# Optimization experiments

Hardware: AMD Instinct MI355X
Metric: run time of the kernel (lower is better)

Reference implementation:

```python
import jax, jax.numpy as jnp
import numpy as np

# Static graph layout: B equal-sized graphs of N nodes, DEG random edges per node.
B, N, DEG = 128, 1024, 16
F_IN, H, C = 2, 64, 2
RATIO = 0.8
E = B * N * DEG
K1 = int(np.ceil(RATIO * N))      # 820
K2 = int(np.ceil(RATIO * K1))     # 656
K3 = int(np.ceil(RATIO * K2))     # 525


def setup_inputs() -> dict:
    key = jax.random.key(0)
    ks = jax.random.split(key, 24)
    x = jax.random.normal(ks[0], (B * N, F_IN), jnp.float32)
    edge_attr = jax.random.uniform(ks[1], (E,), jnp.float32)
    # per-graph random endpoints, offset so edges stay inside each graph
    local = jax.random.randint(ks[2], (2, B, N * DEG), 0, N)
    edge_index = (local + (jnp.arange(B) * N)[None, :, None]).reshape(2, E)

    def lin(k, i, o):
        return jax.random.normal(k, (i, o), jnp.float32) / np.sqrt(i)

    def bias(k, o):
        return jax.random.normal(k, (o,), jnp.float32) * 0.01

    return {
        "x": x, "edge_attr": edge_attr,
        "W1": lin(ks[3], F_IN, H), "b1": bias(ks[4], H),
        "Wp1": lin(ks[5], H, 1), "bp1": bias(ks[6], 1),
        "W2": lin(ks[7], H, H), "b2": bias(ks[8], H),
        "Wp2": lin(ks[9], H, 1), "bp2": bias(ks[10], 1),
        "W3": lin(ks[11], H, H), "b3": bias(ks[12], H),
        "Wp3": lin(ks[13], H, 1), "bp3": bias(ks[14], 1),
        "Wl1": lin(ks[15], 2 * H, H), "bl1": bias(ks[16], H),
        "Wl2": lin(ks[17], H, H // 2), "bl2": bias(ks[18], H // 2),
        "Wl3": lin(ks[19], H // 2, C), "bl3": bias(ks[20], C),
        "edge_index": edge_index,
    }


def gcn(x, src, dst, w, W, b):
    """PyG GCNConv with gcn_norm (self-loops weight 1)."""
    h = x @ W                                       # [BN, out]
    deg = jnp.zeros((x.shape[0],), x.dtype).at[dst].add(w) + 1.0
    dinv = jax.lax.rsqrt(deg)
    norm = dinv[src] * w * dinv[dst]                # [E]
    out = jnp.zeros_like(h).at[dst].add(norm[:, None] * h[src])
    out = out + (dinv * dinv)[:, None] * h          # self-loop term
    return out + b


def sagpool(x, alive, src, dst, Wp, bp, k):
    """SAGPool: unweighted GCN scoring, per-graph top-k, x <- x * tanh(score).
    Removed nodes/edges are kept as masked (alive=False) slots -> static shapes."""
    we = (alive[src] & alive[dst]).astype(x.dtype)
    score = gcn(x, src, dst, we, Wp, bp)[:, 0]      # [BN]
    s = jnp.where(alive, score, -jnp.inf).reshape(B, N)
    _, idx = jax.lax.top_k(s, k)                    # [B, k]
    alive_new = jnp.zeros((B, N), bool).at[jnp.arange(B)[:, None], idx].set(True).reshape(-1)
    xn = jnp.where(alive_new[:, None], x * jnp.tanh(score)[:, None], 0.0)
    return xn, alive_new


def readout(x, alive):
    """concat(global_max_pool, global_mean_pool) over alive nodes per graph."""
    xr = x.reshape(B, N, -1)
    m = alive.reshape(B, N, 1)
    mx = jnp.max(jnp.where(m, xr, -jnp.inf), axis=1)
    mn = jnp.sum(jnp.where(m, xr, 0.0), axis=1) / jnp.sum(m, axis=1).astype(x.dtype)
    return jnp.concatenate([mx, mn], axis=1)        # [B, 2*H]


def _forward(x, edge_attr, W1, b1, Wp1, bp1, W2, b2, Wp2, bp2, W3, b3, Wp3, bp3,
             Wl1, bl1, Wl2, bl2, Wl3, bl3, edge_index):
    src, dst = edge_index[0], edge_index[1]
    h = jax.nn.relu(gcn(x, src, dst, edge_attr, W1, b1))
    h, a1 = sagpool(h, jnp.ones((B * N,), bool), src, dst, Wp1, bp1, K1)
    x1 = readout(h, a1)

    ea1 = edge_attr * (a1[src] & a1[dst]).astype(x.dtype)
    h = jax.nn.relu(gcn(h, src, dst, ea1, W2, b2))
    h, a2 = sagpool(h, a1, src, dst, Wp2, bp2, K2)
    x2 = readout(h, a2)

    # conv3 is called WITHOUT edge_weight -> surviving edges get weight 1
    ea2 = (a2[src] & a2[dst]).astype(x.dtype)
    h = jax.nn.relu(gcn(h, src, dst, ea2, W3, b3))
    h, a3 = sagpool(h, a2, src, dst, Wp3, bp3, K3)
    x3 = readout(h, a3)

    g = x1 + x2 + x3
    g = jax.nn.relu(g @ Wl1 + bl1)                  # dropout: eval mode (identity)
    g = jax.nn.relu(g @ Wl2 + bl2)
    return jax.nn.log_softmax(g @ Wl3 + bl3, axis=-1)


def reference(x, edge_attr, W1, b1, Wp1, bp1, W2, b2, Wp2, bp2, W3, b3, Wp3, bp3,
              Wl1, bl1, Wl2, bl2, Wl3, bl3, edge_index):
    return _forward(x, edge_attr, W1, b1, Wp1, bp1, W2, b2, Wp2, bp2, W3, b3,
                    Wp3, bp3, Wl1, bl1, Wl2, bl2, Wl3, bl3, edge_index)
```

## Files before the change

### kernel.cpp

```cpp
#include <hip/hip_runtime.h>
#include <math.h>

#define NB 128
#define NN 1024
#define BNODES (NB*NN)
#define NE 2097152
#define EPG (NE/NB)
#define EPT (EPG/NN)
#define FH 64
#define KK1 820
#define KK2 656
#define KK3 525

__global__ __launch_bounds__(1024) void k_csr(const int* __restrict__ ei,
                                              const float* __restrict__ ea,
                                              int* __restrict__ rowptr,
                                              int2* __restrict__ csr_sw,
                                              int* __restrict__ aliveA,
                                              float* __restrict__ dinvW,
                                              float* __restrict__ dinvU) {
  extern __shared__ int2 lcsr[];
  __shared__ int cnt[NN];
  __shared__ int cur[NN];
  __shared__ float wsum[NN];
  int b = blockIdx.x, t = threadIdx.x;
  int node = b*NN + t;
  aliveA[node] = 1;
  cnt[t] = 0;
  wsum[t] = 0.f;
  __syncthreads();
  int ebase = b*EPG;
  int se[EPT]; int de[EPT]; float we[EPT];
  #pragma unroll
  for (int i = 0; i < EPT; ++i) {
    int e = ebase + i*NN + t;
    se[i] = ei[e];
    de[i] = ei[NE + e] - b*NN;
    we[i] = ea[e];
    atomicAdd(&cnt[de[i]], 1);
    atomicAdd(&wsum[de[i]], we[i]);
  }
  __syncthreads();
  int v = cnt[t];
  for (int off = 1; off < NN; off <<= 1) {
    int u = (t >= off) ? cnt[t - off] : 0;
    __syncthreads();
    cnt[t] += u;
    __syncthreads();
  }
  int excl = cnt[t] - v;
  rowptr[node] = ebase + excl;
  cur[t] = excl;
  dinvW[node] = rsqrtf(1.f + wsum[t]);
  dinvU[node] = rsqrtf(1.f + (float)v);
  if (b == NB-1 && t == NN-1) rowptr[BNODES] = NE;
  __syncthreads();
  #pragma unroll
  for (int i = 0; i < EPT; ++i) {
    int pos = atomicAdd(&cur[de[i]], 1);
    lcsr[pos] = make_int2(se[i], __float_as_int(we[i]));
  }
  __syncthreads();
  float4* dst4 = (float4*)(csr_sw + ebase);
  const float4* src4 = (const float4*)lcsr;
  #pragma unroll
  for (int i = 0; i < EPG/2/NN; ++i)
    dst4[i*NN + t] = src4[i*NN + t];
}

template<int MODE>
__global__ void k_degs(const int* __restrict__ rowptr, const int2* __restrict__ csr_sw,
                       const int* __restrict__ alive,
                       float* __restrict__ dinvW, float* __restrict__ dinvU) {
  int t = threadIdx.x;
  int l16 = t & 15;
  int d = blockIdx.x*16 + (t >> 4);
  int r0 = rowptr[d], r1 = rowptr[d+1];
  float sW = 0.f, sU = 0.f;
  for (int base = r0; base < r1; base += 16) {
    if (base + l16 < r1) {
      int2 p = csr_sw[base + l16];
      if (alive[p.x]) { sW += (MODE == 2) ? 1.f : __int_as_float(p.y); sU += 1.f; }
    }
  }
  #pragma unroll
  for (int off = 8; off; off >>= 1) {
    sW += __shfl_xor(sW, off, 16);
    sU += __shfl_xor(sU, off, 16);
  }
  if (l16 == 0) {
    bool dA = (alive[d] != 0);
    dinvW[d] = dA ? rsqrtf(1.f + sW) : 0.f;
    dinvU[d] = dA ? rsqrtf(1.f + sU) : 0.f;
  }
}

__global__ void k_lin1(const float* __restrict__ x, const float* __restrict__ W,
                       float* __restrict__ h) {
  int i = blockIdx.x*256 + threadIdx.x;
  if (i >= BNODES*FH) return;
  int node = i >> 6, f = i & 63;
  h[i] = x[2*node]*W[f] + x[2*node+1]*W[FH + f];
}

__global__ void k_lin64(const float* __restrict__ hA, const float* __restrict__ tm,
                        const float* __restrict__ W, float* __restrict__ hB) {
  __shared__ float sX[64][65];
  __shared__ float sW[64*64];
  int t = threadIdx.x;
  for (int i = t; i < 1024; i += 256) ((float4*)sW)[i] = ((const float4*)W)[i];
  int nb = blockIdx.x * 64;
  #pragma unroll
  for (int i = 0; i < 16; ++i) {
    int gidx = (nb << 6) + i*256 + t;
    int node = gidx >> 6, f = gidx & 63;
    sX[node - nb][f] = hA[gidx] * tm[node];
  }
  __syncthreads();
  int node = t >> 2;
  int f0 = (t & 3) * 16;
  float4 a0 = {0,0,0,0}, a1 = a0, a2 = a0, a3 = a0;
  #pragma unroll 4
  for (int k = 0; k < 64; ++k) {
    float xv = sX[node][k];
    const float4 w0 = *(const float4*)&sW[k*64 + f0];
    const float4 w1 = *(const float4*)&sW[k*64 + f0 + 4];
    const float4 w2 = *(const float4*)&sW[k*64 + f0 + 8];
    const float4 w3 = *(const float4*)&sW[k*64 + f0 + 12];
    a0.x = fmaf(xv, w0.x, a0.x); a0.y = fmaf(xv, w0.y, a0.y);
    a0.z = fmaf(xv, w0.z, a0.z); a0.w = fmaf(xv, w0.w, a0.w);
    a1.x = fmaf(xv, w1.x, a1.x); a1.y = fmaf(xv, w1.y, a1.y);
    a1.z = fmaf(xv, w1.z, a1.z); a1.w = fmaf(xv, w1.w, a1.w);
    a2.x = fmaf(xv, w2.x, a2.x); a2.y = fmaf(xv, w2.y, a2.y);
    a2.z = fmaf(xv, w2.z, a2.z); a2.w = fmaf(xv, w2.w, a2.w);
    a3.x = fmaf(xv, w3.x, a3.x); a3.y = fmaf(xv, w3.y, a3.y);
    a3.z = fmaf(xv, w3.z, a3.z); a3.w = fmaf(xv, w3.w, a3.w);
  }
  float4* dst = (float4*)(hB + (size_t)(nb + node)*FH + f0);
  dst[0] = a0; dst[1] = a1; dst[2] = a2; dst[3] = a3;
}

template<int MODE>
__global__ __launch_bounds__(1024) void k_gath(
    const int* __restrict__ rowptr, const int2* __restrict__ csr_sw,
    const float* __restrict__ dinvW, const float* __restrict__ hB,
    const float* __restrict__ bias, const float* __restrict__ Wp,
    float* __restrict__ hA, float* __restrict__ qpart) {
  extern __shared__ float sHB[];
  __shared__ float sDW[NN];
  __shared__ float sWp[32];
  __shared__ float sB[32];
  int b = blockIdx.x >> 1, half = blockIdx.x & 1;
  int t = threadIdx.x, l8 = t & 7;
  int gbase = b*NN;
  sDW[t] = dinvW[gbase + t];
  if (t < 32) { sWp[t] = Wp[half*32 + t]; sB[t] = bias[half*32 + t]; }
  const float4* hB4 = (const float4*)hB;
  float4* sHB4 = (float4*)sHB;
  #pragma unroll
  for (int i = 0; i < 8; ++i) {
    int idx = i*1024 + t;
    int n = idx >> 3, j = idx & 7;
    sHB4[n*8 + j] = hB4[(size_t)(gbase + n)*16 + half*8 + j];
  }
  __syncthreads();
  float4 bv = ((const float4*)sB)[l8];
  float4 wp = ((const float4*)sWp)[l8];
  #pragma unroll 1
  for (int pass = 0; pass < 8; ++pass) {
    int n = pass*128 + (t >> 3);
    int gn = gbase + n;
    float dd = sDW[n];
    float4 hv = sHB4[n*8 + l8];
    float dd2 = dd*dd;
    float4 acc;
    acc.x = fmaf(dd2, hv.x, bv.x);
    acc.y = fmaf(dd2, hv.y, bv.y);
    acc.z = fmaf(dd2, hv.z, bv.z);
    acc.w = fmaf(dd2, hv.w, bv.w);
    int r0 = rowptr[gn], r1 = rowptr[gn+1];
    for (int base = r0; base < r1; base += 8) {
      int sj = 0; float cj = 0.f;
      if (base + l8 < r1) {
        int2 p = csr_sw[base + l8];
        sj = p.x - gbase;
        float w = (MODE == 2) ? 1.f : __int_as_float(p.y);
        cj = sDW[sj] * w * dd;
      }
      #pragma unroll
      for (int j = 0; j < 8; ++j) {
        int s   = __shfl(sj, j, 8);
        float c = __shfl(cj, j, 8);
        float4 v = sHB4[s*8 + l8];
        acc.x = fmaf(c, v.x, acc.x);
        acc.y = fmaf(c, v.y, acc.y);
        acc.z = fmaf(c, v.z, acc.z);
        acc.w = fmaf(c, v.w, acc.w);
      }
    }
    acc.x = fmaxf(acc.x, 0.f); acc.y = fmaxf(acc.y, 0.f);
    acc.z = fmaxf(acc.z, 0.f); acc.w = fmaxf(acc.w, 0.f);
    ((float4*)hA)[(size_t)gn*16 + half*8 + l8] = acc;
    float dot = acc.x*wp.x + acc.y*wp.y + acc.z*wp.z + acc.w*wp.w;
    dot += __shfl_xor(dot, 4, 8);
    dot += __shfl_xor(dot, 2, 8);
    dot += __shfl_xor(dot, 1, 8);
    if (l8 == 0) qpart[half*BNODES + gn] = dot;
  }
}

__global__ void k_qfin(const float* __restrict__ dinvU, const float* __restrict__ qp,
                       float* __restrict__ q) {
  int i = blockIdx.x*256 + threadIdx.x;
  if (i < BNODES) q[i] = dinvU[i]*(qp[i] + qp[BNODES + i]);
}

__global__ void k_score(const int* __restrict__ rowptr, const int2* __restrict__ csr_sw,
                        const float* __restrict__ dinvU, const float* __restrict__ q,
                        const float* __restrict__ bp, float* __restrict__ score) {
  int t = threadIdx.x;
  int l16 = t & 15;
  int d = blockIdx.x*16 + (t >> 4);
  float du = dinvU[d];
  float sum = 0.f;
  if (du != 0.f) {
    int r0 = rowptr[d], r1 = rowptr[d+1];
    for (int base = r0; base < r1; base += 16)
      if (base + l16 < r1) sum += q[csr_sw[base + l16].x];
  }
  #pragma unroll
  for (int off = 8; off; off >>= 1) sum += __shfl_xor(sum, off, 16);
  if (l16 == 0) score[d] = bp[0] + du*(q[d] + sum);
}

__global__ void k_topk(const float* __restrict__ score,
                       const int* __restrict__ alive, int k,
                       float* __restrict__ tm, int* __restrict__ aliveNext) {
  __shared__ float sc[NN];
  int b = blockIdx.x >> 2, p = blockIdx.x & 3;
  int t = threadIdx.x;
  int gbase = b*NN;
  #pragma unroll
  for (int i = 0; i < 4; ++i) {
    int n = i*256 + t;
    sc[n] = alive[gbase + n] ? score[gbase + n] : -INFINITY;
  }
  __syncthreads();
  int n = p*256 + t;
  int node = gbase + n;
  float me = sc[n];
  float raw = score[node];
  int rank = 0;
  const float4* sc4 = (const float4*)sc;
  for (int j4 = 0; j4 < NN/4; ++j4) {
    float4 o = sc4[j4];
    int jb = j4*4;
    rank += (o.x > me) || (o.x == me && jb+0 < n);
    rank += (o.y > me) || (o.y == me && jb+1 < n);
    rank += (o.z > me) || (o.z == me && jb+2 < n);
    rank += (o.w > me) || (o.w == me && jb+3 < n);
  }
  int sel = (rank < k) ? 1 : 0;
  aliveNext[node] = sel;
  tm[node] = sel ? tanhf(raw) : 0.f;
}

__global__ void k_sread(const float* __restrict__ hA, const float* __restrict__ tm,
                        const int* __restrict__ aliveN,
                        float* __restrict__ pmax, float* __restrict__ psum) {
  __shared__ float rm[4][FH], rs[4][FH];
  int b = blockIdx.x >> 2, p = blockIdx.x & 3;
  int t = threadIdx.x, f = t & 63, r = t >> 6;
  float mx = -INFINITY, sm = 0.f;
  for (int i = 0; i < 64; ++i) {
    int n = p*256 + i*4 + r;
    int node = b*NN + n;
    float v = hA[(size_t)node*FH + f] * tm[node];
    if (aliveN[node]) { mx = fmaxf(mx, v); sm += v; }
  }
  rm[r][f] = mx; rs[r][f] = sm;
  __syncthreads();
  if (t < FH) {
    float m2 = fmaxf(fmaxf(rm[0][t], rm[1][t]), fmaxf(rm[2][t], rm[3][t]));
    float s2 = rs[0][t] + rs[1][t] + rs[2][t] + rs[3][t];
    pmax[(b*4 + p)*FH + t] = m2;
    psum[(b*4 + p)*FH + t] = s2;
  }
}

__global__ void k_mlp(const float* __restrict__ pmax, const float* __restrict__ psum,
                      const float* __restrict__ Wl1, const float* __restrict__ bl1,
                      const float* __restrict__ Wl2, const float* __restrict__ bl2,
                      const float* __restrict__ Wl3, const float* __restrict__ bl3,
                      float* __restrict__ out) {
  __shared__ float sg[2*FH];
  __shared__ float l1[FH];
  __shared__ float l2[FH/2];
  __shared__ float l3[2];
  int b = blockIdx.x, t = threadIdx.x;
  const float kf[3] = {(float)KK1, (float)KK2, (float)KK3};
  float gm = 0.f, gs = 0.f;
  #pragma unroll
  for (int l = 0; l < 3; ++l) {
    const float* pm = pmax + (size_t)l*NB*4*FH + (b*4)*FH;
    const float* ps = psum + (size_t)l*NB*4*FH + (b*4)*FH;
    float mm = -INFINITY, ss = 0.f;
    #pragma unroll
    for (int p = 0; p < 4; ++p) {
      mm = fmaxf(mm, pm[p*FH + t]);
      ss += ps[p*FH + t];
    }
    gm += mm;
    gs += ss / kf[l];
  }
  sg[t] = gm;
  sg[FH + t] = gs;
  __syncthreads();
  float acc = bl1[t];
  #pragma unroll
  for (int k = 0; k < 2*FH; ++k) acc = fmaf(sg[k], Wl1[k*FH + t], acc);
  l1[t] = fmaxf(acc, 0.f);
  __syncthreads();
  if (t < 32) {
    float a2 = bl2[t];
    #pragma unroll
    for (int k = 0; k < FH; ++k) a2 = fmaf(l1[k], Wl2[k*32 + t], a2);
    l2[t] = fmaxf(a2, 0.f);
  }
  __syncthreads();
  if (t < 2) {
    float a3 = bl3[t];
    #pragma unroll
    for (int k = 0; k < 32; ++k) a3 = fmaf(l2[k], Wl3[k*2 + t], a3);
    l3[t] = a3;
  }
  __syncthreads();
  if (t == 0) {
    float m = fmaxf(l3[0], l3[1]);
    float lse = m + logf(expf(l3[0]-m) + expf(l3[1]-m));
    out[b*2+0] = l3[0] - lse;
    out[b*2+1] = l3[1] - lse;
  }
}

extern "C" void kernel_launch(void* const* d_in, const int* in_sizes, int n_in,
                              void* d_out, int out_size, void* d_ws, size_t ws_size,
                              hipStream_t stream) {
  const float* x   = (const float*)d_in[0];
  const float* ea  = (const float*)d_in[1];
  const float* W1  = (const float*)d_in[2];
  const float* b1  = (const float*)d_in[3];
  const float* Wp1 = (const float*)d_in[4];
  const float* bp1 = (const float*)d_in[5];
  const float* W2  = (const float*)d_in[6];
  const float* b2  = (const float*)d_in[7];
  const float* Wp2 = (const float*)d_in[8];
  const float* bp2 = (const float*)d_in[9];
  const float* W3  = (const float*)d_in[10];
  const float* b3  = (const float*)d_in[11];
  const float* Wp3 = (const float*)d_in[12];
  const float* bp3 = (const float*)d_in[13];
  const float* Wl1 = (const float*)d_in[14];
  const float* bl1 = (const float*)d_in[15];
  const float* Wl2 = (const float*)d_in[16];
  const float* bl2 = (const float*)d_in[17];
  const float* Wl3 = (const float*)d_in[18];
  const float* bl3 = (const float*)d_in[19];
  const int*   ei  = (const int*)d_in[20];
  float* out = (float*)d_out;

  int2* csr_sw = (int2*)d_ws;
  float* hA    = (float*)(csr_sw + NE);
  float* hB    = hA + (size_t)BNODES*FH;
  float* dinvW = hB + (size_t)BNODES*FH;
  float* dinvU = dinvW + BNODES;
  float* q     = dinvU + BNODES;
  float* qpart = q + BNODES;
  float* score = qpart + 2*BNODES;
  float* tm    = score + BNODES;
  float* pmax  = tm + BNODES;
  float* psum  = pmax + 3*NB*4*FH;
  int* aliveA  = (int*)(psum + 3*NB*4*FH);
  int* aliveB  = aliveA + BNODES;
  int* rowptr  = aliveB + BNODES;

  const int TB = 256;
  const int gG  = BNODES / 16;
  const int gNH = BNODES*FH / TB;
  const int gL  = BNODES / 64;
  const int gN  = BNODES / TB;
  const size_t gathLds = (size_t)NN*32*sizeof(float);

  k_csr<<<NB, 1024, EPG*sizeof(int2), stream>>>(ei, ea, rowptr, csr_sw, aliveA,
                                                dinvW, dinvU);

  k_lin1<<<gNH, TB, 0, stream>>>(x, W1, hB);
  k_gath<0><<<NB*2, 1024, gathLds, stream>>>(rowptr, csr_sw, dinvW, hB, b1, Wp1, hA, qpart);
  k_qfin<<<gN, TB, 0, stream>>>(dinvU, qpart, q);
  k_score<<<gG, TB, 0, stream>>>(rowptr, csr_sw, dinvU, q, bp1, score);
  k_topk<<<NB*4, TB, 0, stream>>>(score, aliveA, KK1, tm, aliveB);
  k_sread<<<NB*4, TB, 0, stream>>>(hA, tm, aliveB, pmax, psum);

  k_degs<1><<<gG, TB, 0, stream>>>(rowptr, csr_sw, aliveB, dinvW, dinvU);
  k_lin64<<<gL, TB, 0, stream>>>(hA, tm, W2, hB);
  k_gath<1><<<NB*2, 1024, gathLds, stream>>>(rowptr, csr_sw, dinvW, hB, b2, Wp2, hA, qpart);
  k_qfin<<<gN, TB, 0, stream>>>(dinvU, qpart, q);
  k_score<<<gG, TB, 0, stream>>>(rowptr, csr_sw, dinvU, q, bp2, score);
  k_topk<<<NB*4, TB, 0, stream>>>(score, aliveB, KK2, tm, aliveA);
  k_sread<<<NB*4, TB, 0, stream>>>(hA, tm, aliveA, pmax + NB*4*FH, psum + NB*4*FH);

  k_degs<2><<<gG, TB, 0, stream>>>(rowptr, csr_sw, aliveA, dinvW, dinvU);
  k_lin64<<<gL, TB, 0, stream>>>(hA, tm, W3, hB);
  k_gath<2><<<NB*2, 1024, gathLds, stream>>>(rowptr, csr_sw, dinvW, hB, b3, Wp3, hA, qpart);
  k_qfin<<<gN, TB, 0, stream>>>(dinvU, qpart, q);
  k_score<<<gG, TB, 0, stream>>>(rowptr, csr_sw, dinvU, q, bp3, score);
  k_topk<<<NB*4, TB, 0, stream>>>(score, aliveA, KK3, tm, aliveB);
  k_sread<<<NB*4, TB, 0, stream>>>(hA, tm, aliveB, pmax + 2*NB*4*FH, psum + 2*NB*4*FH);

  k_mlp<<<NB, FH, 0, stream>>>(pmax, psum, Wl1, bl1, Wl2, bl2, Wl3, bl3, out);
}
```

Baseline: 452.0 us.

## Fuse GCN pipeline stages into per-graph pool and readout-linear kernels

```diff
diff --git a/kernel.cpp b/kernel.cpp
--- a/kernel.cpp
+++ b/kernel.cpp
@@ -16,7 +16,6 @@
                                               const float* __restrict__ ea,
                                               int* __restrict__ rowptr,
                                               int2* __restrict__ csr_sw,
-                                              int* __restrict__ aliveA,
                                               float* __restrict__ dinvW,
                                               float* __restrict__ dinvU) {
   extern __shared__ int2 lcsr[];
@@ -25,7 +24,6 @@
   __shared__ float wsum[NN];
   int b = blockIdx.x, t = threadIdx.x;
   int node = b*NN + t;
-  aliveA[node] = 1;
   cnt[t] = 0;
   wsum[t] = 0.f;
   __syncthreads();
@@ -68,100 +66,43 @@
     dst4[i*NN + t] = src4[i*NN + t];
 }
 
-template<int MODE>
-__global__ void k_degs(const int* __restrict__ rowptr, const int2* __restrict__ csr_sw,
-                       const int* __restrict__ alive,
-                       float* __restrict__ dinvW, float* __restrict__ dinvU) {
-  int t = threadIdx.x;
-  int l16 = t & 15;
-  int d = blockIdx.x*16 + (t >> 4);
-  int r0 = rowptr[d], r1 = rowptr[d+1];
-  float sW = 0.f, sU = 0.f;
-  for (int base = r0; base < r1; base += 16) {
-    if (base + l16 < r1) {
-      int2 p = csr_sw[base + l16];
-      if (alive[p.x]) { sW += (MODE == 2) ? 1.f : __int_as_float(p.y); sU += 1.f; }
-    }
-  }
-  #pragma unroll
-  for (int off = 8; off; off >>= 1) {
-    sW += __shfl_xor(sW, off, 16);
-    sU += __shfl_xor(sU, off, 16);
-  }
-  if (l16 == 0) {
-    bool dA = (alive[d] != 0);
-    dinvW[d] = dA ? rsqrtf(1.f + sW) : 0.f;
-    dinvU[d] = dA ? rsqrtf(1.f + sU) : 0.f;
-  }
-}
-
-__global__ void k_lin1(const float* __restrict__ x, const float* __restrict__ W,
-                       float* __restrict__ h) {
-  int i = blockIdx.x*256 + threadIdx.x;
-  if (i >= BNODES*FH) return;
-  int node = i >> 6, f = i & 63;
-  h[i] = x[2*node]*W[f] + x[2*node+1]*W[FH + f];
-}
-
-__global__ void k_lin64(const float* __restrict__ hA, const float* __restrict__ tm,
-                        const float* __restrict__ W, float* __restrict__ hB) {
-  __shared__ float sX[64][65];
-  __shared__ float sW[64*64];
-  int t = threadIdx.x;
-  for (int i = t; i < 1024; i += 256) ((float4*)sW)[i] = ((const float4*)W)[i];
-  int nb = blockIdx.x * 64;
-  #pragma unroll
-  for (int i = 0; i < 16; ++i) {
-    int gidx = (nb << 6) + i*256 + t;
-    int node = gidx >> 6, f = gidx & 63;
-    sX[node - nb][f] = hA[gidx] * tm[node];
-  }
-  __syncthreads();
-  int node = t >> 2;
-  int f0 = (t & 3) * 16;
-  float4 a0 = {0,0,0,0}, a1 = a0, a2 = a0, a3 = a0;
-  #pragma unroll 4
-  for (int k = 0; k < 64; ++k) {
-    float xv = sX[node][k];
-    const float4 w0 = *(const float4*)&sW[k*64 + f0];
-    const float4 w1 = *(const float4*)&sW[k*64 + f0 + 4];
-    const float4 w2 = *(const float4*)&sW[k*64 + f0 + 8];
-    const float4 w3 = *(const float4*)&sW[k*64 + f0 + 12];
-    a0.x = fmaf(xv, w0.x, a0.x); a0.y = fmaf(xv, w0.y, a0.y);
-    a0.z = fmaf(xv, w0.z, a0.z); a0.w = fmaf(xv, w0.w, a0.w);
-    a1.x = fmaf(xv, w1.x, a1.x); a1.y = fmaf(xv, w1.y, a1.y);
-    a1.z = fmaf(xv, w1.z, a1.z); a1.w = fmaf(xv, w1.w, a1.w);
-    a2.x = fmaf(xv, w2.x, a2.x); a2.y = fmaf(xv, w2.y, a2.y);
-    a2.z = fmaf(xv, w2.z, a2.z); a2.w = fmaf(xv, w2.w, a2.w);
-    a3.x = fmaf(xv, w3.x, a3.x); a3.y = fmaf(xv, w3.y, a3.y);
-    a3.z = fmaf(xv, w3.z, a3.z); a3.w = fmaf(xv, w3.w, a3.w);
-  }
-  float4* dst = (float4*)(hB + (size_t)(nb + node)*FH + f0);
-  dst[0] = a0; dst[1] = a1; dst[2] = a2; dst[3] = a3;
-}
-
-template<int MODE>
-__global__ __launch_bounds__(1024) void k_gath(
+template<int MODE, bool L1S>
+__global__ __launch_bounds__(1024, 4) void k_gath(
     const int* __restrict__ rowptr, const int2* __restrict__ csr_sw,
-    const float* __restrict__ dinvW, const float* __restrict__ hB,
+    const float* __restrict__ dinvW, const float* __restrict__ src,
+    const float* __restrict__ Wl,
     const float* __restrict__ bias, const float* __restrict__ Wp,
     float* __restrict__ hA, float* __restrict__ qpart) {
   extern __shared__ float sHB[];
   __shared__ float sDW[NN];
   __shared__ float sWp[32];
   __shared__ float sB[32];
+  __shared__ float sW1[64];
   int b = blockIdx.x >> 1, half = blockIdx.x & 1;
   int t = threadIdx.x, l8 = t & 7;
   int gbase = b*NN;
   sDW[t] = dinvW[gbase + t];
   if (t < 32) { sWp[t] = Wp[half*32 + t]; sB[t] = bias[half*32 + t]; }
-  const float4* hB4 = (const float4*)hB;
   float4* sHB4 = (float4*)sHB;
-  #pragma unroll
-  for (int i = 0; i < 8; ++i) {
-    int idx = i*1024 + t;
-    int n = idx >> 3, j = idx & 7;
-    sHB4[n*8 + j] = hB4[(size_t)(gbase + n)*16 + half*8 + j];
+  if (L1S) {
+    if (t < 32) { sW1[t] = Wl[half*32 + t]; sW1[32 + t] = Wl[64 + half*32 + t]; }
+    __syncthreads();
+    #pragma unroll
+    for (int i = 0; i < 32; ++i) {
+      int el = i*1024 + t;
+      int n = el >> 5, ff = el & 31;
+      float x0 = src[(size_t)(gbase + n)*2];
+      float x1 = src[(size_t)(gbase + n)*2 + 1];
+      sHB[n*32 + ff] = x0*sW1[ff] + x1*sW1[32 + ff];
+    }
+  } else {
+    const float4* hB4 = (const float4*)src;
+    #pragma unroll
+    for (int i = 0; i < 8; ++i) {
+      int idx = i*1024 + t;
+      int n = idx >> 3, j = idx & 7;
+      sHB4[n*8 + j] = hB4[(size_t)(gbase + n)*16 + half*8 + j];
+    }
   }
   __syncthreads();
   float4 bv = ((const float4*)sB)[l8];
@@ -187,15 +128,19 @@
         float w = (MODE == 2) ? 1.f : __int_as_float(p.y);
         cj = sDW[sj] * w * dd;
       }
+      float4 v[8];
       #pragma unroll
       for (int j = 0; j < 8; ++j) {
-        int s   = __shfl(sj, j, 8);
+        int s = __shfl(sj, j, 8);
+        v[j] = sHB4[s*8 + l8];
+      }
+      #pragma unroll
+      for (int j = 0; j < 8; ++j) {
         float c = __shfl(cj, j, 8);
-        float4 v = sHB4[s*8 + l8];
-        acc.x = fmaf(c, v.x, acc.x);
-        acc.y = fmaf(c, v.y, acc.y);
-        acc.z = fmaf(c, v.z, acc.z);
-        acc.w = fmaf(c, v.w, acc.w);
+        acc.x = fmaf(c, v[j].x, acc.x);
+        acc.y = fmaf(c, v[j].y, acc.y);
+        acc.z = fmaf(c, v[j].z, acc.z);
+        acc.w = fmaf(c, v[j].w, acc.w);
       }
     }
     acc.x = fmaxf(acc.x, 0.f); acc.y = fmaxf(acc.y, 0.f);
@@ -209,82 +154,148 @@
   }
 }
 
-__global__ void k_qfin(const float* __restrict__ dinvU, const float* __restrict__ qp,
-                       float* __restrict__ q) {
-  int i = blockIdx.x*256 + threadIdx.x;
-  if (i < BNODES) q[i] = dinvU[i]*(qp[i] + qp[BNODES + i]);
-}
-
-__global__ void k_score(const int* __restrict__ rowptr, const int2* __restrict__ csr_sw,
-                        const float* __restrict__ dinvU, const float* __restrict__ q,
-                        const float* __restrict__ bp, float* __restrict__ score) {
-  int t = threadIdx.x;
-  int l16 = t & 15;
-  int d = blockIdx.x*16 + (t >> 4);
-  float du = dinvU[d];
-  float sum = 0.f;
-  if (du != 0.f) {
-    int r0 = rowptr[d], r1 = rowptr[d+1];
+template<int NEXTMODE>
+__global__ __launch_bounds__(1024) void k_pool(
+    const int* __restrict__ rowptr, const int2* __restrict__ csr_sw,
+    const float* __restrict__ qpart, const float* __restrict__ bp, int k,
+    float* __restrict__ tm, int* __restrict__ aliveN,
+    float* dinvW, float* dinvU) {
+  __shared__ float sq[NN];
+  __shared__ float sdU[NN];
+  __shared__ float sc[NN];
+  __shared__ float sraw[NN];
+  __shared__ int ssel[NN];
+  int b = blockIdx.x, t = threadIdx.x;
+  int gbase = b*NN;
+  float du = dinvU[gbase + t];
+  sdU[t] = du;
+  sq[t] = du * (qpart[gbase + t] + qpart[BNODES + gbase + t]);
+  __syncthreads();
+  int l16 = t & 15, g = t >> 4;
+  float bpv = bp[0];
+  for (int i = 0; i < 16; ++i) {
+    int n = g*16 + i;
+    int gn = gbase + n;
+    int r0 = rowptr[gn], r1 = rowptr[gn+1];
+    float sum = 0.f;
     for (int base = r0; base < r1; base += 16)
-      if (base + l16 < r1) sum += q[csr_sw[base + l16].x];
-  }
-  #pragma unroll
-  for (int off = 8; off; off >>= 1) sum += __shfl_xor(sum, off, 16);
-  if (l16 == 0) score[d] = bp[0] + du*(q[d] + sum);
-}
-
-__global__ void k_topk(const float* __restrict__ score,
-                       const int* __restrict__ alive, int k,
-                       float* __restrict__ tm, int* __restrict__ aliveNext) {
-  __shared__ float sc[NN];
-  int b = blockIdx.x >> 2, p = blockIdx.x & 3;
-  int t = threadIdx.x;
-  int gbase = b*NN;
-  #pragma unroll
-  for (int i = 0; i < 4; ++i) {
-    int n = i*256 + t;
-    sc[n] = alive[gbase + n] ? score[gbase + n] : -INFINITY;
-  }
-  __syncthreads();
-  int n = p*256 + t;
-  int node = gbase + n;
-  float me = sc[n];
-  float raw = score[node];
+      if (base + l16 < r1) sum += sq[csr_sw[base + l16].x - gbase];
+    #pragma unroll
+    for (int off = 8; off; off >>= 1) sum += __shfl_xor(sum, off, 16);
+    if (l16 == 0) {
+      float dun = sdU[n];
+      float raw = bpv + dun*(sq[n] + sum);
+      sraw[n] = raw;
+      sc[n] = (dun != 0.f) ? raw : -INFINITY;
+    }
+  }
+  __syncthreads();
+  float me = sc[t];
   int rank = 0;
   const float4* sc4 = (const float4*)sc;
   for (int j4 = 0; j4 < NN/4; ++j4) {
     float4 o = sc4[j4];
     int jb = j4*4;
-    rank += (o.x > me) || (o.x == me && jb+0 < n);
-    rank += (o.y > me) || (o.y == me && jb+1 < n);
-    rank += (o.z > me) || (o.z == me && jb+2 < n);
-    rank += (o.w > me) || (o.w == me && jb+3 < n);
+    rank += (o.x > me) || (o.x == me && jb+0 < t);
+    rank += (o.y > me) || (o.y == me && jb+1 < t);
+    rank += (o.z > me) || (o.z == me && jb+2 < t);
+    rank += (o.w > me) || (o.w == me && jb+3 < t);
   }
   int sel = (rank < k) ? 1 : 0;
-  aliveNext[node] = sel;
-  tm[node] = sel ? tanhf(raw) : 0.f;
-}
-
-__global__ void k_sread(const float* __restrict__ hA, const float* __restrict__ tm,
-                        const int* __restrict__ aliveN,
-                        float* __restrict__ pmax, float* __restrict__ psum) {
+  ssel[t] = sel;
+  aliveN[gbase + t] = sel;
+  tm[gbase + t] = sel ? tanhf(sraw[t]) : 0.f;
+  __syncthreads();
+  if (NEXTMODE != 0) {
+    for (int i = 0; i < 16; ++i) {
+      int n = g*16 + i;
+      int gn = gbase + n;
+      int r0 = rowptr[gn], r1 = rowptr[gn+1];
+      float sW = 0.f, sU = 0.f;
+      for (int base = r0; base < r1; base += 16)
+        if (base + l16 < r1) {
+          int2 p = csr_sw[base + l16];
+          if (ssel[p.x - gbase]) {
+            sW += (NEXTMODE == 2) ? 1.f : __int_as_float(p.y);
+            sU += 1.f;
+          }
+        }
+      #pragma unroll
+      for (int off = 8; off; off >>= 1) {
+        sW += __shfl_xor(sW, off, 16);
+        sU += __shfl_xor(sU, off, 16);
+      }
+      if (l16 == 0) {
+        bool dA = ssel[n] != 0;
+        dinvW[gn] = dA ? rsqrtf(1.f + sW) : 0.f;
+        dinvU[gn] = dA ? rsqrtf(1.f + sU) : 0.f;
+      }
+    }
+  }
+}
+
+template<bool DOLIN>
+__global__ void k_srl(const float* __restrict__ hA, const float* __restrict__ tm,
+                      const int* __restrict__ aliveN, const float* __restrict__ W,
+                      float* __restrict__ hB,
+                      float* __restrict__ pmax, float* __restrict__ psum) {
+  __shared__ float sX[64][65];
+  __shared__ float sW[64*64];
+  __shared__ int sAl[64];
   __shared__ float rm[4][FH], rs[4][FH];
-  int b = blockIdx.x >> 2, p = blockIdx.x & 3;
-  int t = threadIdx.x, f = t & 63, r = t >> 6;
-  float mx = -INFINITY, sm = 0.f;
-  for (int i = 0; i < 64; ++i) {
-    int n = p*256 + i*4 + r;
-    int node = b*NN + n;
-    float v = hA[(size_t)node*FH + f] * tm[node];
-    if (aliveN[node]) { mx = fmaxf(mx, v); sm += v; }
-  }
-  rm[r][f] = mx; rs[r][f] = sm;
+  int t = threadIdx.x;
+  int blk = blockIdx.x;
+  int nb = blk*64;
+  if (DOLIN)
+    for (int i = t; i < 1024; i += 256) ((float4*)sW)[i] = ((const float4*)W)[i];
+  if (t < 64) sAl[t] = aliveN[nb + t];
+  #pragma unroll
+  for (int i = 0; i < 16; ++i) {
+    int gidx = (nb << 6) + i*256 + t;
+    int node = gidx >> 6, f = gidx & 63;
+    sX[node - nb][f] = hA[gidx] * tm[node];
+  }
+  __syncthreads();
+  {
+    int f = t & 63, r = t >> 6;
+    float mx = -INFINITY, sm = 0.f;
+    #pragma unroll
+    for (int i = 0; i < 16; ++i) {
+      int n = r + i*4;
+      float v = sX[n][f];
+      if (sAl[n]) { mx = fmaxf(mx, v); sm += v; }
+    }
+    rm[r][f] = mx; rs[r][f] = sm;
+  }
   __syncthreads();
   if (t < FH) {
     float m2 = fmaxf(fmaxf(rm[0][t], rm[1][t]), fmaxf(rm[2][t], rm[3][t]));
     float s2 = rs[0][t] + rs[1][t] + rs[2][t] + rs[3][t];
-    pmax[(b*4 + p)*FH + t] = m2;
-    psum[(b*4 + p)*FH + t] = s2;
+    pmax[blk*FH + t] = m2;
+    psum[blk*FH + t] = s2;
+  }
+  if (DOLIN) {
+    int node = t >> 2;
+    int f0 = (t & 3) * 16;
+    float4 a0 = {0,0,0,0}, a1 = a0, a2 = a0, a3 = a0;
+    #pragma unroll 4
+    for (int k = 0; k < 64; ++k) {
+      float xv = sX[node][k];
+      const float4 w0 = *(const float4*)&sW[k*64 + f0];
+      const float4 w1 = *(const float4*)&sW[k*64 + f0 + 4];
+      const float4 w2 = *(const float4*)&sW[k*64 + f0 + 8];
+      const float4 w3 = *(const float4*)&sW[k*64 + f0 + 12];
+      a0.x = fmaf(xv, w0.x, a0.x); a0.y = fmaf(xv, w0.y, a0.y);
+      a0.z = fmaf(xv, w0.z, a0.z); a0.w = fmaf(xv, w0.w, a0.w);
+      a1.x = fmaf(xv, w1.x, a1.x); a1.y = fmaf(xv, w1.y, a1.y);
+      a1.z = fmaf(xv, w1.z, a1.z); a1.w = fmaf(xv, w1.w, a1.w);
+      a2.x = fmaf(xv, w2.x, a2.x); a2.y = fmaf(xv, w2.y, a2.y);
+      a2.z = fmaf(xv, w2.z, a2.z); a2.w = fmaf(xv, w2.w, a2.w);
+      a3.x = fmaf(xv, w3.x, a3.x); a3.y = fmaf(xv, w3.y, a3.y);
+      a3.z = fmaf(xv, w3.z, a3.z); a3.w = fmaf(xv, w3.w, a3.w);
+    }
+    float4* dst = (float4*)(hB + (size_t)(nb + node)*FH + f0);
+    dst[0] = a0; dst[1] = a1; dst[2] = a2; dst[3] = a3;
   }
 }
 
@@ -302,11 +313,11 @@
   float gm = 0.f, gs = 0.f;
   #pragma unroll
   for (int l = 0; l < 3; ++l) {
-    const float* pm = pmax + (size_t)l*NB*4*FH + (b*4)*FH;
-    const float* ps = psum + (size_t)l*NB*4*FH + (b*4)*FH;
+    const float* pm = pmax + (size_t)l*NB*16*FH + (b*16)*FH;
+    const float* ps = psum + (size_t)l*NB*16*FH + (b*16)*FH;
     float mm = -INFINITY, ss = 0.f;
     #pragma unroll
-    for (int p = 0; p < 4; ++p) {
+    for (int p = 0; p < 16; ++p) {
       mm = fmaxf(mm, pm[p*FH + t]);
       ss += ps[p*FH + t];
     }
@@ -374,48 +385,29 @@
   float* hB    = hA + (size_t)BNODES*FH;
   float* dinvW = hB + (size_t)BNODES*FH;
   float* dinvU = dinvW + BNODES;
-  float* q     = dinvU + BNODES;
-  float* qpart = q + BNODES;
-  float* score = qpart + 2*BNODES;
-  float* tm    = score + BNODES;
+  float* qpart = dinvU + BNODES;
+  float* tm    = qpart + 2*BNODES;
   float* pmax  = tm + BNODES;
-  float* psum  = pmax + 3*NB*4*FH;
-  int* aliveA  = (int*)(psum + 3*NB*4*FH);
-  int* aliveB  = aliveA + BNODES;
-  int* rowptr  = aliveB + BNODES;
-
-  const int TB = 256;
-  const int gG  = BNODES / 16;
-  const int gNH = BNODES*FH / TB;
-  const int gL  = BNODES / 64;
-  const int gN  = BNODES / TB;
+  float* psum  = pmax + 3*NB*16*FH;
+  int* aliveN  = (int*)(psum + 3*NB*16*FH);
+  int* rowptr  = aliveN + BNODES;
+
   const size_t gathLds = (size_t)NN*32*sizeof(float);
-
-  k_csr<<<NB, 1024, EPG*sizeof(int2), stream>>>(ei, ea, rowptr, csr_sw, aliveA,
-                                                dinvW, dinvU);
-
-  k_lin1<<<gNH, TB, 0, stream>>>(x, W1, hB);
-  k_gath<0><<<NB*2, 1024, gathLds, stream>>>(rowptr, csr_sw, dinvW, hB, b1, Wp1, hA, qpart);
-  k_qfin<<<gN, TB, 0, stream>>>(dinvU, qpart, q);
-  k_score<<<gG, TB, 0, stream>>>(rowptr, csr_sw, dinvU, q, bp1, score);
-  k_topk<<<NB*4, TB, 0, stream>>>(score, aliveA, KK1, tm, aliveB);
-  k_sread<<<NB*4, TB, 0, stream>>>(hA, tm, aliveB, pmax, psum);
-
-  k_degs<1><<<gG, TB, 0, stream>>>(rowptr, csr_sw, aliveB, dinvW, dinvU);
-  k_lin64<<<gL, TB, 0, stream>>>(hA, tm, W2, hB);
-  k_gath<1><<<NB*2, 1024, gathLds, stream>>>(rowptr, csr_sw, dinvW, hB, b2, Wp2, hA, qpart);
-  k_qfin<<<gN, TB, 0, stream>>>(dinvU, qpart, q);
-  k_score<<<gG, TB, 0, stream>>>(rowptr, csr_sw, dinvU, q, bp2, score);
-  k_topk<<<NB*4, TB, 0, stream>>>(score, aliveB, KK2, tm, aliveA);
-  k_sread<<<NB*4, TB, 0, stream>>>(hA, tm, aliveA, pmax + NB*4*FH, psum + NB*4*FH);
-
-  k_degs<2><<<gG, TB, 0, stream>>>(rowptr, csr_sw, aliveA, dinvW, dinvU);
-  k_lin64<<<gL, TB, 0, stream>>>(hA, tm, W3, hB);
-  k_gath<2><<<NB*2, 1024, gathLds, stream>>>(rowptr, csr_sw, dinvW, hB, b3, Wp3, hA, qpart);
-  k_qfin<<<gN, TB, 0, stream>>>(dinvU, qpart, q);
-  k_score<<<gG, TB, 0, stream>>>(rowptr, csr_sw, dinvU, q, bp3, score);
-  k_topk<<<NB*4, TB, 0, stream>>>(score, aliveA, KK3, tm, aliveB);
-  k_sread<<<NB*4, TB, 0, stream>>>(hA, tm, aliveB, pmax + 2*NB*4*FH, psum + 2*NB*4*FH);
+  const int gS = BNODES/64;
+
+  k_csr<<<NB, 1024, EPG*sizeof(int2), stream>>>(ei, ea, rowptr, csr_sw, dinvW, dinvU);
+
+  k_gath<0,true><<<NB*2, 1024, gathLds, stream>>>(rowptr, csr_sw, dinvW, x, W1, b1, Wp1, hA, qpart);
+  k_pool<1><<<NB, 1024, 0, stream>>>(rowptr, csr_sw, qpart, bp1, KK1, tm, aliveN, dinvW, dinvU);
+  k_srl<true><<<gS, 256, 0, stream>>>(hA, tm, aliveN, W2, hB, pmax, psum);
+
+  k_gath<1,false><<<NB*2, 1024, gathLds, stream>>>(rowptr, csr_sw, dinvW, hB, W1, b2, Wp2, hA, qpart);
+  k_pool<2><<<NB, 1024, 0, stream>>>(rowptr, csr_sw, qpart, bp2, KK2, tm, aliveN, dinvW, dinvU);
+  k_srl<true><<<gS, 256, 0, stream>>>(hA, tm, aliveN, W3, hB, pmax + NB*16*FH, psum + NB*16*FH);
+
+  k_gath<2,false><<<NB*2, 1024, gathLds, stream>>>(rowptr, csr_sw, dinvW, hB, W1, b3, Wp3, hA, qpart);
+  k_pool<0><<<NB, 1024, 0, stream>>>(rowptr, csr_sw, qpart, bp3, KK3, tm, aliveN, dinvW, dinvU);
+  k_srl<false><<<gS, 256, 0, stream>>>(hA, tm, aliveN, W3, hB, pmax + 2*NB*16*FH, psum + 2*NB*16*FH);
 
   k_mlp<<<NB, FH, 0, stream>>>(pmax, psum, Wl1, bl1, Wl2, bl2, Wl3, bl3, out);
 }
```

New measurement: 445.0 us. No clear change (-1.5%).
